# Kernel tuning notes

Measured on AMD Instinct MI355X. Metric: run time of the kernel, lower is better.

## Reference

```python
import jax, jax.numpy as jnp
import numpy as np

EPS = 1e-12  # torch F.normalize default eps


def _l2norm(x):
    n = jnp.linalg.norm(x, axis=-1, keepdims=True)
    return x / jnp.maximum(n, EPS)


def setup_inputs() -> dict:
    key = jax.random.key(0)
    k1, k2 = jax.random.split(key)
    B, D = 8192, 1024
    img_emb = jax.random.normal(k1, (B, D), dtype=jnp.float32)
    txt_emb = jax.random.normal(k2, (B, D), dtype=jnp.float32)
    t_prime = jnp.asarray(np.log(1.0 / 0.1), dtype=jnp.float32)  # log(1/temperature_init)
    bias = jnp.asarray(-10.0, dtype=jnp.float32)
    return {"img_emb": img_emb, "txt_emb": txt_emb, "t_prime": t_prime, "bias": bias}


def reference(img_emb, txt_emb, t_prime, bias):
    img = _l2norm(img_emb)
    txt = _l2norm(txt_emb)
    t = jnp.minimum(jnp.exp(t_prime), 100.0)
    logits = jnp.einsum('id,jd->ij', img, txt) * t + bias  # [B, B]
    B = img.shape[0]
    # STANDARD mode: labels = 2*I - 1
    labels = 2.0 * jnp.eye(B, dtype=logits.dtype) - 1.0
    loss = -jnp.sum(jax.nn.log_sigmoid(labels * logits)) / B
    return loss
```

## Files before the change

kernel.cpp:

```cpp
#include <hip/hip_runtime.h>
#include <hip/hip_bf16.h>

#define B_SZ 8192
#define D_SZ 1024

typedef __attribute__((ext_vector_type(4))) float floatx4;
typedef __attribute__((ext_vector_type(8))) int   int8v;
typedef __attribute__((ext_vector_type(4))) int   int4v;

__device__ __forceinline__ void glds16(const void* g, void* l) {
    __builtin_amdgcn_global_load_lds(
        (const __attribute__((address_space(1))) void*)g,
        (__attribute__((address_space(3))) void*)l, 16, 0, 0);
}

__global__ __launch_bounds__(256) void norm_cast_fp8(
    const float* __restrict__ img, const float* __restrict__ txt,
    unsigned char* __restrict__ imgQ, unsigned char* __restrict__ txtQ)
{
    const int lane = threadIdx.x & 63;
    int w = blockIdx.x * 4 + (threadIdx.x >> 6);
    const float* src; unsigned char* dst;
    if (w < B_SZ) { src = img + (size_t)w * D_SZ; dst = imgQ + (size_t)w * D_SZ; }
    else { w -= B_SZ; src = txt + (size_t)w * D_SZ; dst = txtQ + (size_t)w * D_SZ; }

    float4 v[4];
    float ss = 0.0f;
    #pragma unroll
    for (int i = 0; i < 4; ++i) {
        v[i] = ((const float4*)src)[lane + 64 * i];
        ss += v[i].x*v[i].x + v[i].y*v[i].y + v[i].z*v[i].z + v[i].w*v[i].w;
    }
    #pragma unroll
    for (int off = 1; off < 64; off <<= 1) ss += __shfl_xor(ss, off, 64);
    const float scale = 1.0f / fmaxf(sqrtf(ss), 1e-12f);

    #pragma unroll
    for (int i = 0; i < 4; ++i) {
        int packed = 0;
        packed = __builtin_amdgcn_cvt_pk_fp8_f32(v[i].x * scale, v[i].y * scale, packed, false);
        packed = __builtin_amdgcn_cvt_pk_fp8_f32(v[i].z * scale, v[i].w * scale, packed, true);
        ((int*)dst)[lane + 64 * i] = packed;
    }
}

__global__ __launch_bounds__(256) void siglip_gemm_loss_fp8(
    const unsigned char* __restrict__ A,
    const unsigned char* __restrict__ Bt,
    const float* __restrict__ tp, const float* __restrict__ bp,
    float* __restrict__ out)
{
    __shared__ __align__(16) unsigned char As[128 * 128];
    __shared__ __align__(16) unsigned char Bs[128 * 128];

    const int tid  = threadIdx.x;
    const int lane = tid & 63;
    const int wave = tid >> 6;
    const int wm = wave & 1, wn = wave >> 1;
    const int bi = blockIdx.x * 128;
    const int bj = blockIdx.y * 128;
    const int quad = lane >> 4;
    const int l16  = lane & 15;
    const int sw   = l16 & 7;

    floatx4 acc[4][4];
    #pragma unroll
    for (int i = 0; i < 4; ++i)
        #pragma unroll
        for (int j = 0; j < 4; ++j)
            acc[i][j] = (floatx4){0.f, 0.f, 0.f, 0.f};

    for (int k0 = 0; k0 < D_SZ; k0 += 128) {
        #pragma unroll
        for (int it = 0; it < 4; ++it) {
            int s = tid + it * 256;
            int row = s >> 3, p = s & 7;
            int g = p ^ (row & 7);
            glds16(A  + ((size_t)(bi + row) * D_SZ + k0 + g * 16), As + s * 16);
            glds16(Bt + ((size_t)(bj + row) * D_SZ + k0 + g * 16), Bs + s * 16);
        }
        __syncthreads();

        int8v af[4], bf[4];
        #pragma unroll
        for (int mt = 0; mt < 4; ++mt) {
            int r = wm * 64 + mt * 16 + l16;
            int4v lo = *(const int4v*)(As + r * 128 + (((quad*2)    ) ^ sw) * 16);
            int4v hi = *(const int4v*)(As + r * 128 + (((quad*2) + 1) ^ sw) * 16);
            af[mt][0]=lo[0]; af[mt][1]=lo[1]; af[mt][2]=lo[2]; af[mt][3]=lo[3];
            af[mt][4]=hi[0]; af[mt][5]=hi[1]; af[mt][6]=hi[2]; af[mt][7]=hi[3];
        }
        #pragma unroll
        for (int nt = 0; nt < 4; ++nt) {
            int r = wn * 64 + nt * 16 + l16;
            int4v lo = *(const int4v*)(Bs + r * 128 + (((quad*2)    ) ^ sw) * 16);
            int4v hi = *(const int4v*)(Bs + r * 128 + (((quad*2) + 1) ^ sw) * 16);
            bf[nt][0]=lo[0]; bf[nt][1]=lo[1]; bf[nt][2]=lo[2]; bf[nt][3]=lo[3];
            bf[nt][4]=hi[0]; bf[nt][5]=hi[1]; bf[nt][6]=hi[2]; bf[nt][7]=hi[3];
        }
        #pragma unroll
        for (int mt = 0; mt < 4; ++mt)
            #pragma unroll
            for (int nt = 0; nt < 4; ++nt)
                acc[mt][nt] = __builtin_amdgcn_mfma_scale_f32_16x16x128_f8f6f4(
                    af[mt], bf[nt], acc[mt][nt],
                    0, 0,
                    0, 127,
                    0, 127);
        __syncthreads();
    }

    const float t    = fminf(__expf(tp[0]), 100.0f);
    const float bias = bp[0];
    float lsum = 0.0f;
    #pragma unroll
    for (int mt = 0; mt < 4; ++mt) {
        #pragma unroll
        for (int nt = 0; nt < 4; ++nt) {
            const int jj = bj + wn * 64 + nt * 16 + l16;
            #pragma unroll
            for (int r = 0; r < 4; ++r) {
                const int ii = bi + wm * 64 + mt * 16 + quad * 4 + r;
                float logit = fmaf(acc[mt][nt][r], t, bias);
                float z = (ii == jj) ? logit : -logit;
                float e = __expf(-fabsf(z));
                lsum += fmaxf(-z, 0.0f) + __logf(1.0f + e);
            }
        }
    }
    #pragma unroll
    for (int off = 32; off > 0; off >>= 1) lsum += __shfl_down(lsum, off, 64);

    __shared__ float red[4];
    if (lane == 0) red[wave] = lsum;
    __syncthreads();
    if (tid == 0)
        atomicAdd(out, (red[0] + red[1] + red[2] + red[3]) * (1.0f / (float)B_SZ));
}

extern "C" void kernel_launch(void* const* d_in, const int* in_sizes, int n_in,
                              void* d_out, int out_size, void* d_ws, size_t ws_size,
                              hipStream_t stream) {
    const float* img = (const float*)d_in[0];
    const float* txt = (const float*)d_in[1];
    const float* tp  = (const float*)d_in[2];
    const float* bp  = (const float*)d_in[3];
    float* out = (float*)d_out;

    unsigned char* imgQ = (unsigned char*)d_ws;
    unsigned char* txtQ = imgQ + (size_t)B_SZ * D_SZ;

    hipMemsetAsync(out, 0, sizeof(float), stream);
    norm_cast_fp8<<<(2 * B_SZ) / 4, 256, 0, stream>>>(img, txt, imgQ, txtQ);
    dim3 grid(B_SZ / 128, B_SZ / 128);
    siglip_gemm_loss_fp8<<<grid, 256, 0, stream>>>(imgQ, txtQ, tp, bp, out);
}
```

Measured before the change: 203.3 us.

## Overlap next K-tile global-to-LDS load with MFMA compute and split LDS layout

Restructures the FP8 GEMM main loop so each K-tile's fragments are read into registers, a barrier is taken, and then the next tile's global_load_lds is issued before the MFMAs run. Load latency can then overlap with matrix math. The LDS tile is split into two 64-byte-wide halves with a new XOR swizzle to keep bank conflicts low, and launch_bounds now requests 3 blocks per CU for occupancy. Risks include holding all fragments in registers while the next load is in flight, and correctness of the new swizzle mapping.

```diff
diff --git a/kernel.cpp b/kernel.cpp
--- a/kernel.cpp
+++ b/kernel.cpp
@@ -44,14 +44,14 @@
     }
 }
 
-__global__ __launch_bounds__(256) void siglip_gemm_loss_fp8(
+__global__ __launch_bounds__(256, 3) void siglip_gemm_loss_fp8(
     const unsigned char* __restrict__ A,
     const unsigned char* __restrict__ Bt,
     const float* __restrict__ tp, const float* __restrict__ bp,
     float* __restrict__ out)
 {
-    __shared__ __align__(16) unsigned char As[128 * 128];
-    __shared__ __align__(16) unsigned char Bs[128 * 128];
+    __shared__ __align__(16) unsigned char As[2][128 * 64];
+    __shared__ __align__(16) unsigned char Bs[2][128 * 64];
 
     const int tid  = threadIdx.x;
     const int lane = tid & 63;
@@ -61,7 +61,6 @@
     const int bj = blockIdx.y * 128;
     const int quad = lane >> 4;
     const int l16  = lane & 15;
-    const int sw   = l16 & 7;
 
     floatx4 acc[4][4];
     #pragma unroll
@@ -70,34 +69,55 @@
         for (int j = 0; j < 4; ++j)
             acc[i][j] = (floatx4){0.f, 0.f, 0.f, 0.f};
 
-    for (int k0 = 0; k0 < D_SZ; k0 += 128) {
+    auto stage = [&](int k0) {
         #pragma unroll
-        for (int it = 0; it < 4; ++it) {
+        for (int it = 0; it < 2; ++it) {
             int s = tid + it * 256;
-            int row = s >> 3, p = s & 7;
-            int g = p ^ (row & 7);
-            glds16(A  + ((size_t)(bi + row) * D_SZ + k0 + g * 16), As + s * 16);
-            glds16(Bt + ((size_t)(bj + row) * D_SZ + k0 + g * 16), Bs + s * 16);
+            int row = s >> 2, p = s & 3;
+            int g = p ^ ((row >> 1) & 3);
+            const unsigned char* ga = A  + ((size_t)(bi + row) * D_SZ + k0 + g * 16);
+            const unsigned char* gb = Bt + ((size_t)(bj + row) * D_SZ + k0 + g * 16);
+            glds16(ga,      As[0] + s * 16);
+            glds16(ga + 64, As[1] + s * 16);
+            glds16(gb,      Bs[0] + s * 16);
+            glds16(gb + 64, Bs[1] + s * 16);
         }
+    };
+
+    const int sw = (l16 >> 1) & 3;
+    const int hsel = quad >> 1;
+    const int q2 = (quad & 1) * 2;
+    const int p0 = (q2    ) ^ sw;
+    const int p1 = (q2 + 1) ^ sw;
+
+    stage(0);
+
+    for (int kk = 0; kk < D_SZ / 128; ++kk) {
         __syncthreads();
 
         int8v af[4], bf[4];
         #pragma unroll
         for (int mt = 0; mt < 4; ++mt) {
             int r = wm * 64 + mt * 16 + l16;
-            int4v lo = *(const int4v*)(As + r * 128 + (((quad*2)    ) ^ sw) * 16);
-            int4v hi = *(const int4v*)(As + r * 128 + (((quad*2) + 1) ^ sw) * 16);
+            int4v lo = *(const int4v*)(As[hsel] + r * 64 + p0 * 16);
+            int4v hi = *(const int4v*)(As[hsel] + r * 64 + p1 * 16);
             af[mt][0]=lo[0]; af[mt][1]=lo[1]; af[mt][2]=lo[2]; af[mt][3]=lo[3];
             af[mt][4]=hi[0]; af[mt][5]=hi[1]; af[mt][6]=hi[2]; af[mt][7]=hi[3];
         }
         #pragma unroll
         for (int nt = 0; nt < 4; ++nt) {
             int r = wn * 64 + nt * 16 + l16;
-            int4v lo = *(const int4v*)(Bs + r * 128 + (((quad*2)    ) ^ sw) * 16);
-            int4v hi = *(const int4v*)(Bs + r * 128 + (((quad*2) + 1) ^ sw) * 16);
+            int4v lo = *(const int4v*)(Bs[hsel] + r * 64 + p0 * 16);
+            int4v hi = *(const int4v*)(Bs[hsel] + r * 64 + p1 * 16);
             bf[nt][0]=lo[0]; bf[nt][1]=lo[1]; bf[nt][2]=lo[2]; bf[nt][3]=lo[3];
             bf[nt][4]=hi[0]; bf[nt][5]=hi[1]; bf[nt][6]=hi[2]; bf[nt][7]=hi[3];
         }
+
+        __syncthreads();
+
+        if (kk + 1 < D_SZ / 128)
+            stage((kk + 1) * 128);
+
         #pragma unroll
         for (int mt = 0; mt < 4; ++mt)
             #pragma unroll
@@ -107,7 +127,6 @@
                     0, 0,
                     0, 127,
                     0, 127);
-        __syncthreads();
     }
 
     const float t    = fminf(__expf(tp[0]), 100.0f);
```

Result: faster. 192.3 us (-5.4%).

## Pre-swizzle FP8 operands into MFMA fragment layout and load directly from global

Applied to the files above, without the earlier changes.

The normalize/cast kernel now writes each 16-row group in the exact per-lane MFMA fragment order, staging through shared memory. The GEMM then drops its LDS staging and barriers and loads A/B fragments straight from global memory with contiguous 32-byte per-lane reads. The output memset is folded into the first kernel. The goal is to remove LDS traffic and synchronisation from the GEMM main loop, at the cost of relying on L2/cache reuse across waves and blocks and of having no explicit software pipelining.

```diff
diff --git a/kernel.cpp b/kernel.cpp
--- a/kernel.cpp
+++ b/kernel.cpp
@@ -8,51 +8,64 @@
 typedef __attribute__((ext_vector_type(8))) int   int8v;
 typedef __attribute__((ext_vector_type(4))) int   int4v;
 
-__device__ __forceinline__ void glds16(const void* g, void* l) {
-    __builtin_amdgcn_global_load_lds(
-        (const __attribute__((address_space(1))) void*)g,
-        (__attribute__((address_space(3))) void*)l, 16, 0, 0);
-}
 
-__global__ __launch_bounds__(256) void norm_cast_fp8(
+__global__ __launch_bounds__(256) void norm_cast_fp8t(
     const float* __restrict__ img, const float* __restrict__ txt,
-    unsigned char* __restrict__ imgQ, unsigned char* __restrict__ txtQ)
+    unsigned char* __restrict__ imgT, unsigned char* __restrict__ txtT,
+    float* __restrict__ out)
 {
-    const int lane = threadIdx.x & 63;
-    int w = blockIdx.x * 4 + (threadIdx.x >> 6);
+    if (blockIdx.x == 0 && threadIdx.x == 0) *out = 0.0f;
+
+    int b = blockIdx.x;
     const float* src; unsigned char* dst;
-    if (w < B_SZ) { src = img + (size_t)w * D_SZ; dst = imgQ + (size_t)w * D_SZ; }
-    else { w -= B_SZ; src = txt + (size_t)w * D_SZ; dst = txtQ + (size_t)w * D_SZ; }
+    if (b < B_SZ / 16) { src = img + (size_t)b * 16 * D_SZ; dst = imgT + (size_t)b * 16 * D_SZ; }
+    else { b -= B_SZ / 16; src = txt + (size_t)b * 16 * D_SZ; dst = txtT + (size_t)b * 16 * D_SZ; }
 
-    float4 v[4];
+    const int t = threadIdx.x;
+    const int r = t >> 4;
+    const int m = t & 15;
+
+    float4 v[16];
     float ss = 0.0f;
     #pragma unroll
-    for (int i = 0; i < 4; ++i) {
-        v[i] = ((const float4*)src)[lane + 64 * i];
-        ss += v[i].x*v[i].x + v[i].y*v[i].y + v[i].z*v[i].z + v[i].w*v[i].w;
+    for (int j = 0; j < 16; ++j) {
+        v[j] = ((const float4*)src)[r * 256 + m + 16 * j];
+        ss += v[j].x*v[j].x + v[j].y*v[j].y + v[j].z*v[j].z + v[j].w*v[j].w;
     }
     #pragma unroll
-    for (int off = 1; off < 64; off <<= 1) ss += __shfl_xor(ss, off, 64);
+    for (int off = 1; off < 16; off <<= 1) ss += __shfl_xor(ss, off, 64);
     const float scale = 1.0f / fmaxf(sqrtf(ss), 1e-12f);
 
+    __shared__ unsigned char P[16 * 1024];
     #pragma unroll
-    for (int i = 0; i < 4; ++i) {
+    for (int j = 0; j < 16; ++j) {
         int packed = 0;
-        packed = __builtin_amdgcn_cvt_pk_fp8_f32(v[i].x * scale, v[i].y * scale, packed, false);
-        packed = __builtin_amdgcn_cvt_pk_fp8_f32(v[i].z * scale, v[i].w * scale, packed, true);
-        ((int*)dst)[lane + 64 * i] = packed;
+        packed = __builtin_amdgcn_cvt_pk_fp8_f32(v[j].x * scale, v[j].y * scale, packed, false);
+        packed = __builtin_amdgcn_cvt_pk_fp8_f32(v[j].z * scale, v[j].w * scale, packed, true);
+        *(int*)(P + r * 1024 + m * 4 + 64 * j) = packed;
+    }
+    __syncthreads();
+
+    const int c = t >> 5, s = t & 31;
+    #pragma unroll
+    for (int h = 0; h < 2; ++h) {
+        const int sl = s + h * 32;
+        const int l16 = sl & 15, quad = sl >> 4;
+        const unsigned char* p_ = P + l16 * 1024 + c * 128 + quad * 32;
+        int4v w0 = *(const int4v*)(p_);
+        int4v w1 = *(const int4v*)(p_ + 16);
+        unsigned char* gp = dst + c * 2048 + sl * 32;
+        *(int4v*)(gp)      = w0;
+        *(int4v*)(gp + 16) = w1;
     }
 }
 
-__global__ __launch_bounds__(256) void siglip_gemm_loss_fp8(
+__global__ __launch_bounds__(256, 2) void siglip_gemm_loss_fp8(
     const unsigned char* __restrict__ A,
     const unsigned char* __restrict__ Bt,
     const float* __restrict__ tp, const float* __restrict__ bp,
     float* __restrict__ out)
 {
-    __shared__ __align__(16) unsigned char As[128 * 128];
-    __shared__ __align__(16) unsigned char Bs[128 * 128];
-
     const int tid  = threadIdx.x;
     const int lane = tid & 63;
     const int wave = tid >> 6;
@@ -61,7 +74,6 @@
     const int bj = blockIdx.y * 128;
     const int quad = lane >> 4;
     const int l16  = lane & 15;
-    const int sw   = l16 & 7;
 
     floatx4 acc[4][4];
     #pragma unroll
@@ -70,44 +82,35 @@
         for (int j = 0; j < 4; ++j)
             acc[i][j] = (floatx4){0.f, 0.f, 0.f, 0.f};
 
-    for (int k0 = 0; k0 < D_SZ; k0 += 128) {
-        #pragma unroll
-        for (int it = 0; it < 4; ++it) {
-            int s = tid + it * 256;
-            int row = s >> 3, p = s & 7;
-            int g = p ^ (row & 7);
-            glds16(A  + ((size_t)(bi + row) * D_SZ + k0 + g * 16), As + s * 16);
-            glds16(Bt + ((size_t)(bj + row) * D_SZ + k0 + g * 16), Bs + s * 16);
-        }
-        __syncthreads();
+    const unsigned char* Ab = A  + (unsigned)((bi >> 4) + wm * 4) * 16384 + lane * 32;
+    const unsigned char* Bb = Bt + (unsigned)((bj >> 4) + wn * 4) * 16384 + lane * 32;
 
-        int8v af[4], bf[4];
+    union frag { int8v v8; struct { int4v lo, hi; } s; };
+
+    #pragma unroll
+    for (int kk = 0; kk < D_SZ / 128; ++kk) {
+        frag af[4], bf[4];
         #pragma unroll
         for (int mt = 0; mt < 4; ++mt) {
-            int r = wm * 64 + mt * 16 + l16;
-            int4v lo = *(const int4v*)(As + r * 128 + (((quad*2)    ) ^ sw) * 16);
-            int4v hi = *(const int4v*)(As + r * 128 + (((quad*2) + 1) ^ sw) * 16);
-            af[mt][0]=lo[0]; af[mt][1]=lo[1]; af[mt][2]=lo[2]; af[mt][3]=lo[3];
-            af[mt][4]=hi[0]; af[mt][5]=hi[1]; af[mt][6]=hi[2]; af[mt][7]=hi[3];
+            const unsigned char* ap = Ab + mt * 16384 + kk * 2048;
+            af[mt].s.lo = *(const int4v*)(ap);
+            af[mt].s.hi = *(const int4v*)(ap + 16);
         }
         #pragma unroll
         for (int nt = 0; nt < 4; ++nt) {
-            int r = wn * 64 + nt * 16 + l16;
-            int4v lo = *(const int4v*)(Bs + r * 128 + (((quad*2)    ) ^ sw) * 16);
-            int4v hi = *(const int4v*)(Bs + r * 128 + (((quad*2) + 1) ^ sw) * 16);
-            bf[nt][0]=lo[0]; bf[nt][1]=lo[1]; bf[nt][2]=lo[2]; bf[nt][3]=lo[3];
-            bf[nt][4]=hi[0]; bf[nt][5]=hi[1]; bf[nt][6]=hi[2]; bf[nt][7]=hi[3];
+            const unsigned char* bp_ = Bb + nt * 16384 + kk * 2048;
+            bf[nt].s.lo = *(const int4v*)(bp_);
+            bf[nt].s.hi = *(const int4v*)(bp_ + 16);
         }
         #pragma unroll
         for (int mt = 0; mt < 4; ++mt)
             #pragma unroll
             for (int nt = 0; nt < 4; ++nt)
                 acc[mt][nt] = __builtin_amdgcn_mfma_scale_f32_16x16x128_f8f6f4(
-                    af[mt], bf[nt], acc[mt][nt],
+                    af[mt].v8, bf[nt].v8, acc[mt][nt],
                     0, 0,
                     0, 127,
                     0, 127);
-        __syncthreads();
     }
 
     const float t    = fminf(__expf(tp[0]), 100.0f);
@@ -147,11 +150,10 @@
     const float* bp  = (const float*)d_in[3];
     float* out = (float*)d_out;
 
-    unsigned char* imgQ = (unsigned char*)d_ws;
-    unsigned char* txtQ = imgQ + (size_t)B_SZ * D_SZ;
+    unsigned char* imgT = (unsigned char*)d_ws;
+    unsigned char* txtT = imgT + (size_t)B_SZ * D_SZ;
 
-    hipMemsetAsync(out, 0, sizeof(float), stream);
-    norm_cast_fp8<<<(2 * B_SZ) / 4, 256, 0, stream>>>(img, txt, imgQ, txtQ);
+    norm_cast_fp8t<<<2 * (B_SZ / 16), 256, 0, stream>>>(img, txt, imgT, txtT, out);
     dim3 grid(B_SZ / 128, B_SZ / 128);
-    siglip_gemm_loss_fp8<<<grid, 256, 0, stream>>>(imgQ, txtQ, tp, bp, out);
+    siglip_gemm_loss_fp8<<<grid, 256, 0, stream>>>(imgT, txtT, tp, bp, out);
 }
```

New measurement: 201.3 us. About the same (-1.0%).
